# Performance work log

Hardware: AMD Instinct MI355X
Metric: run time of the kernel (lower is better)

Reference implementation:

```python
import jax, jax.numpy as jnp
import numpy as np
from jax import lax

FIELD = 32          # backbone receptive-field stride (field_size of ResNet50)
K = 3               # number of anchor sizes
ANCHOR_PX = (32, 64, 96)
POOL = 2
TILES = 3
NMS_IOU = 0.3
R_POST = 512        # post-NMS proposal cap (static shape for jit)
IMG = 1536
MG = IMG // FIELD   # 48x48 feature map
C = 256
HID = 1024


def setup_inputs() -> dict:
    key = jax.random.key(0)
    ks = jax.random.split(key, 6)
    # create_anchors: per feature cell (grid step FIELD) and per anchor size,
    # row = [x_upper_left, y_upper_left, width, height]
    grid = np.arange(MG, dtype=np.float32) * FIELD + FIELD / 2.0  # cell centers
    cy, cx, aa = np.meshgrid(grid, grid, np.array(ANCHOR_PX, np.float32), indexing='ij')
    anchors = np.stack([cx - aa / 2, cy - aa / 2, aa, aa], axis=-1).reshape(-1, 4).astype(np.float32)
    return {
        'features': jax.random.normal(ks[0], (1, MG, MG, C), jnp.float32),
        'anchors': jnp.asarray(anchors),
        'W_obj': jax.random.normal(ks[1], (C, 2 * K), jnp.float32) * 0.1,
        'b_obj': jnp.zeros((2 * K,), jnp.float32),
        'W_reg': jax.random.normal(ks[2], (C, 4 * K), jnp.float32) * 0.01,
        'b_reg': jnp.zeros((4 * K,), jnp.float32),
        'W_fc1': jax.random.normal(ks[3], (TILES * TILES * C, HID), jnp.float32) * 0.02,
        'b_fc1': jnp.zeros((HID,), jnp.float32),
        'W_fc2': jax.random.normal(ks[4], (HID, 4), jnp.float32) * 0.01,
        'b_fc2': jnp.zeros((4,), jnp.float32),
    }


def _map_outputs(out, anchors):
    # out: [M, N, K*D] RPN output; returns [A, D], one row per anchor
    apx = jnp.asarray(ANCHOR_PX, jnp.int32)
    k = jnp.argmax(anchors[:, 3].astype(jnp.int32)[:, None] == apx[None, :], axis=1)
    px = ((anchors[:, 0] + anchors[:, 2] * 0.5) / FIELD).astype(jnp.int32)
    py = ((anchors[:, 1] + anchors[:, 3] * 0.5) / FIELD).astype(jnp.int32)
    M, N, _ = out.shape
    r = out.reshape(M, N, K, -1)
    return r[py, px, k]


def _unparameterize(reg, anchors):
    cxa = anchors[:, 0] + anchors[:, 2] * 0.5
    cya = anchors[:, 1] + anchors[:, 3] * 0.5
    cx = reg[:, 0] * anchors[:, 2] + cxa
    cy = reg[:, 1] * anchors[:, 3] + cya
    w = anchors[:, 2] * jnp.exp(reg[:, 2])
    h = anchors[:, 3] * jnp.exp(reg[:, 3])
    return jnp.stack([cx - w * 0.5, cy - h * 0.5, w, h], axis=1)


def _clip_boxes(b, W, H):
    x1 = jnp.clip(b[:, 0], 0.0, W)
    y1 = jnp.clip(b[:, 1], 0.0, H)
    x2 = jnp.clip(b[:, 0] + b[:, 2], 0.0, W)
    y2 = jnp.clip(b[:, 1] + b[:, 3], 0.0, H)
    return jnp.stack([x1, y1, x2 - x1, y2 - y1], axis=1)


def _pairwise_iou(b):
    x1, y1 = b[:, 0], b[:, 1]
    x2, y2 = b[:, 0] + b[:, 2], b[:, 1] + b[:, 3]
    iw = jnp.maximum(0.0, jnp.minimum(x2[:, None], x2[None, :]) - jnp.maximum(x1[:, None], x1[None, :]))
    ih = jnp.maximum(0.0, jnp.minimum(y2[:, None], y2[None, :]) - jnp.maximum(y1[:, None], y1[None, :]))
    inter = iw * ih
    area = (x2 - x1) * (y2 - y1)
    return inter / (area[:, None] + area[None, :] - inter + 1e-8)


def _roialign(fmap, boxes):
    # fmap: [M, N, C]; boxes: [R, 4] xywh -> [R, TILES, TILES, C]
    M, N, Cc = fmap.shape
    S = TILES * POOL
    offs = (jnp.arange(S, dtype=boxes.dtype) + 0.5) / S
    fx = jnp.clip((boxes[:, 0:1] + offs[None, :] * boxes[:, 2:3]) / FIELD - 0.5, 0.0, N - 1.0)
    fy = jnp.clip((boxes[:, 1:2] + offs[None, :] * boxes[:, 3:4]) / FIELD - 0.5, 0.0, M - 1.0)
    x0 = jnp.floor(fx).astype(jnp.int32); x1 = jnp.minimum(x0 + 1, N - 1); wx = fx - x0
    y0 = jnp.floor(fy).astype(jnp.int32); y1 = jnp.minimum(y0 + 1, M - 1); wy = fy - y0
    def g(yi, xi):
        return fmap[yi[:, :, None], xi[:, None, :]]  # [R, S, S, C]
    wX = wx[:, None, :, None]; wY = wy[:, :, None, None]
    v = (g(y0, x0) * (1 - wY) * (1 - wX) + g(y0, x1) * (1 - wY) * wX
         + g(y1, x0) * wY * (1 - wX) + g(y1, x1) * wY * wX)
    R = boxes.shape[0]
    return v.reshape(R, TILES, POOL, TILES, POOL, Cc).mean(axis=(2, 4))


def reference(features, anchors, W_obj, b_obj, W_reg, b_reg, W_fc1, b_fc1, W_fc2, b_fc2):
    fmap = features[0]  # [M, N, C]
    out_obj = fmap @ W_obj + b_obj   # [M, N, 2K]
    out_reg = fmap @ W_reg + b_reg   # [M, N, 4K]
    rpn_obj = jax.nn.softmax(_map_outputs(out_obj, anchors), axis=1)  # [A, 2]
    rpn_reg = _map_outputs(out_reg, anchors)                          # [A, 4]
    boxes = _clip_boxes(_unparameterize(rpn_reg, anchors), float(IMG), float(IMG))
    scores = rpn_obj[:, 1]
    A = boxes.shape[0]
    # NMS (sequential greedy suppression on score-sorted boxes)
    order = jnp.argsort(-scores)
    iou_mat = lax.stop_gradient(_pairwise_iou(boxes[order]))  # [A, A], index selection is non-diff
    idx = jnp.arange(A)
    def body(i, keep):
        sup = jnp.any((iou_mat[i] > NMS_IOU) & keep & (idx < i))
        return keep.at[i].set(~sup)
    keep = lax.fori_loop(0, A, body, jnp.zeros((A,), bool))
    masked = jnp.where(keep, scores[order], -1e9)
    _, topi = lax.top_k(masked, R_POST)
    sel = order[topi]
    sel_boxes = boxes[sel]
    sel_obj = rpn_obj[sel]
    pooled = _roialign(fmap, sel_boxes)            # [R, TILES, TILES, C]
    flat = pooled.reshape(R_POST, -1)
    h = jax.nn.relu(flat @ W_fc1 + b_fc1)
    align_reg = h @ W_fc2 + b_fc2                  # [R, 4]
    align_boxes = _unparameterize(align_reg, sel_boxes)
    # concat (rpn_obj, rpn_boxes, align_boxes) -> [R, 10]
    return jnp.concatenate([sel_obj, sel_boxes, align_boxes], axis=1)
```

## Files before the change

kernel.cpp:

```cpp
#include <hip/hip_runtime.h>
#include <hip/hip_bf16.h>

typedef unsigned long long ull;

#define MGRID 48
#define CCH   256
#define NCELL 2304
#define NA    6912
#define NW    108
#define NHID  1024
#define KFC   2304
#define RPOST 512
#define IMGF  1536.0f

typedef __attribute__((ext_vector_type(8))) short short8v;
typedef __attribute__((ext_vector_type(4))) float f32x4;

__global__ __launch_bounds__(256) void rpn_head(const float* __restrict__ feat,
    const float* __restrict__ Wobj, const float* __restrict__ bobj,
    const float* __restrict__ Wreg, const float* __restrict__ breg,
    float* __restrict__ rpn){
  int g = blockIdx.x*256 + threadIdx.x;
  int cell = g / 18, o = g % 18;
  const float* x = feat + cell*CCH;
  const float* W; int stride; float acc;
  if (o < 6){ W = Wobj + o; stride = 6;  acc = bobj[o];   }
  else      { W = Wreg + (o-6); stride = 12; acc = breg[o-6]; }
  #pragma unroll 8
  for (int c=0;c<CCH;++c) acc += x[c]*W[c*stride];
  rpn[cell*18 + o] = acc;
}

__global__ __launch_bounds__(256) void anchor_prep(const float* __restrict__ rpn,
    const float* __restrict__ anchors, float* __restrict__ probs,
    float* __restrict__ boxes, ull* __restrict__ keys){
  int a = blockIdx.x*256 + threadIdx.x;
  int cell = a/3, k = a%3;
  const float* rc = rpn + cell*18;
  float l0 = rc[2*k], l1 = rc[2*k+1];
  float m  = fmaxf(l0,l1);
  float e0 = expf(l0-m), e1 = expf(l1-m);
  float s  = e0 + e1;
  float p0 = e0/s, p1 = e1/s;
  probs[a*2+0] = p0; probs[a*2+1] = p1;
  float4 an = ((const float4*)anchors)[a];
  float r0 = rc[6+4*k+0], r1 = rc[6+4*k+1], r2 = rc[6+4*k+2], r3 = rc[6+4*k+3];
  float cxa = an.x + an.z*0.5f, cya = an.y + an.w*0.5f;
  float cx = r0*an.z + cxa, cy = r1*an.w + cya;
  float w  = an.z*expf(r2),  hh = an.w*expf(r3);
  float bx = cx - w*0.5f, by = cy - hh*0.5f;
  float x1 = fminf(fmaxf(bx,      0.0f), IMGF);
  float y1 = fminf(fmaxf(by,      0.0f), IMGF);
  float x2 = fminf(fmaxf(bx + w,  0.0f), IMGF);
  float y2 = fminf(fmaxf(by + hh, 0.0f), IMGF);
  float4 bo; bo.x = x1; bo.y = y1; bo.z = x2 - x1; bo.w = y2 - y1;
  ((float4*)boxes)[a] = bo;
  keys[a] = ((ull)__float_as_uint(p1) << 32) | (unsigned)(NA-1-a);
}

__global__ __launch_bounds__(256) void rank_part(const ull* __restrict__ keys,
                                                 int* __restrict__ part){
  __shared__ ull lk[256];
  int t = threadIdx.x;
  int ib = blockIdx.x, jb = blockIdx.y;
  lk[t] = keys[jb*256 + t];
  int i = ib*256 + t;
  ull ki = keys[i];
  __syncthreads();
  int cnt = 0;
  #pragma unroll 16
  for (int j=0;j<256;++j) cnt += (lk[j] > ki) ? 1 : 0;
  part[jb*NA + i] = cnt;
}

__global__ __launch_bounds__(256) void rank_scatter(const int* __restrict__ part,
    const float* __restrict__ boxes, int* __restrict__ ord, float* __restrict__ sboxes){
  int i = blockIdx.x*256 + threadIdx.x;
  int r = 0;
  #pragma unroll
  for (int jb=0;jb<27;++jb) r += part[jb*NA + i];
  ord[r] = i;
  ((float4*)sboxes)[r] = ((const float4*)boxes)[i];
}

__global__ __launch_bounds__(256) void iou_mask(const float* __restrict__ sboxes,
                                                ull* __restrict__ maskT){
  int gid = blockIdx.x*256 + threadIdx.x;
  int i = gid % NA;
  int w = gid / NA;
  if ((i >> 6) > w + 1) return;
  float4 bi = ((const float4*)sboxes)[i];
  float x1i = bi.x, y1i = bi.y;
  float x2i = bi.x + bi.z, y2i = bi.y + bi.w;
  float ai  = (x2i - x1i) * (y2i - y1i);
  const float4* bj4 = (const float4*)sboxes + w*64;
  ull bits = 0;
  #pragma unroll 8
  for (int jj=0;jj<64;++jj){
    float4 bj = bj4[jj];
    float x1j = bj.x, y1j = bj.y;
    float x2j = bj.x + bj.z, y2j = bj.y + bj.w;
    float aj  = (x2j - x1j) * (y2j - y1j);
    float iw = fmaxf(fminf(x2i,x2j) - fmaxf(x1i,x1j), 0.0f);
    float ih = fmaxf(fminf(y2i,y2j) - fmaxf(y1i,y1j), 0.0f);
    float inter = iw*ih;
    float den = ai + aj - inter + 1e-8f;
    if (inter > 0.3f*den) bits |= (1ull<<jj);
  }
  maskT[(size_t)w*NA + i] = bits;
}

__global__ __launch_bounds__(256) void nms_wcvt(const ull* __restrict__ maskT,
    const int* __restrict__ ord, const float* __restrict__ sboxes,
    const float* __restrict__ probs, const float* __restrict__ Wfc1,
    ushort* __restrict__ Wt, float* __restrict__ out, float* __restrict__ selb){
  if (blockIdx.x != 0){
    __shared__ float tile[32][33];
    int bid = blockIdx.x - 1;
    int bx = bid & 31;
    int by = bid >> 5;
    int tx = threadIdx.x & 31, ty = threadIdx.x >> 5;
    #pragma unroll
    for (int it=0; it<4; ++it)
      tile[ty + 8*it][tx] = Wfc1[(size_t)(by*32 + ty + 8*it)*NHID + bx*32 + tx];
    __syncthreads();
    #pragma unroll
    for (int it=0; it<4; ++it){
      __hip_bfloat16 b = __float2bfloat16(tile[tx][ty + 8*it]);
      Wt[(size_t)(bx*32 + ty + 8*it)*KFC + by*32 + tx] = *(ushort*)&b;
    }
    return;
  }

  __shared__ ull remv[NW];
  __shared__ ull keepw[NW];
  __shared__ ull kb_sh[2];
  __shared__ int selpos[RPOST];
  __shared__ int base_sh[NW];
  __shared__ int cnt_sh, done_sh;
  int t = threadIdx.x;
  if (t < NW){ remv[t] = 0ull; keepw[t] = 0ull; }
  if (t == 0){ cnt_sh = 0; done_sh = 0; kb_sh[0] = 0ull; kb_sh[1] = 0ull; }
  __syncthreads();

  ull dg_cur = 0, srow_cur = 0, kb_prev = 0;
  if (t < 64) dg_cur = maskT[t];

  for (int c = 0; c < NW; ++c){
    if (t < 64){
      ull dg_nxt = 0, srow_nxt = 0;
      if (c+1 < NW){
        dg_nxt   = maskT[(size_t)(c+1)*NA + (size_t)(c+1)*64 + t];
        srow_nxt = maskT[(size_t)c*NA + (size_t)(c+1)*64 + t];
      }
      ull w0 = remv[c];
      bool dec  = ((w0 >> t) & 1ull) || ((srow_cur & kb_prev) != 0ull);
      bool kept = false;
      ull sup = dg_cur & ((1ull << t) - 1ull);
      for (;;){
        ull K = __ballot(kept);
        ull D = __ballot(dec);
        if (D == ~0ull) break;
        if (!dec){
          if (sup & K)                 { dec = true; }
          else if ((sup & ~D) == 0ull) { dec = true; kept = true; }
        }
      }
      ull kb = __ballot(kept);
      int cnt0 = cnt_sh;
      ull below = kb & ((1ull << t) - 1ull);
      int myrank = cnt0 + __popcll(below);
      if (kept && myrank < RPOST) selpos[myrank] = c*64 + t;
      if (t == 0){
        kb_sh[c & 1] = kb;
        keepw[c] = kb;
        int nc = cnt0 + __popcll(kb);
        if (nc >= RPOST){ nc = RPOST; done_sh = 1; }
        cnt_sh = nc;
      }
      kb_prev = kb; dg_cur = dg_nxt; srow_cur = srow_nxt;
    } else {
      int u = t - 64;
      int wp = c + 1 + u;
      if (c >= 1 && wp < NW){
        ull kbp = kb_sh[(c-1) & 1];
        if (kbp){
          const ull* row = maskT + (size_t)wp*NA + (size_t)(c-1)*64;
          ull acc = remv[wp];
          #pragma unroll
          for (int b=0;b<64;++b)
            acc |= (0ull - ((kbp >> b) & 1ull)) & row[b];
          remv[wp] = acc;
        }
      }
    }
    __syncthreads();
    if (done_sh) break;
  }
  __syncthreads();
  int cnt0 = cnt_sh;
  if (cnt0 < RPOST){
    if (t < NW){
      int s = 0;
      for (int w2=0; w2<t; ++w2) s += __popcll(~keepw[w2]);
      base_sh[t] = s;
    }
    __syncthreads();
    for (int p = t; p < NA; p += 256){
      int w2 = p >> 6, b = p & 63;
      ull kw = keepw[w2];
      if (!((kw >> b) & 1ull)){
        int rank = cnt0 + base_sh[w2] + __popcll(~kw & ((1ull << b) - 1ull));
        if (rank < RPOST) selpos[rank] = p;
      }
    }
  }
  __syncthreads();
  for (int s=t; s<RPOST; s+=256){
    int pos = selpos[s];
    int orig = ord[pos];
    float4 b = ((const float4*)sboxes)[pos];
    out[s*10+0] = probs[orig*2+0];
    out[s*10+1] = probs[orig*2+1];
    out[s*10+2] = b.x; out[s*10+3] = b.y; out[s*10+4] = b.z; out[s*10+5] = b.w;
    ((float4*)selb)[s] = b;
  }
}

__global__ __launch_bounds__(256) void roialign(const float* __restrict__ feat,
    const float* __restrict__ selb, __hip_bfloat16* __restrict__ pooled){
  int r = blockIdx.x, c = threadIdx.x;
  float4 b = ((const float4*)selb)[r];
  int x0[6], x1[6], y0[6], y1[6];
  float wx[6], wy[6];
  #pragma unroll
  for (int s=0;s<6;++s){
    float off = ((float)s + 0.5f) / 6.0f;
    float fx = (b.x + off*b.z) / 32.0f - 0.5f;
    fx = fminf(fmaxf(fx, 0.0f), 47.0f);
    int xx0 = (int)floorf(fx);
    x0[s] = xx0; x1[s] = min(xx0+1, 47); wx[s] = fx - (float)xx0;
    float fy = (b.y + off*b.w) / 32.0f - 0.5f;
    fy = fminf(fmaxf(fy, 0.0f), 47.0f);
    int yy0 = (int)floorf(fy);
    y0[s] = yy0; y1[s] = min(yy0+1, 47); wy[s] = fy - (float)yy0;
  }
  #pragma unroll
  for (int ty=0;ty<3;++ty){
    #pragma unroll
    for (int tx=0;tx<3;++tx){
      float sum = 0.0f;
      #pragma unroll
      for (int py=0;py<2;++py){
        #pragma unroll
        for (int px=0;px<2;++px){
          int sy = ty*2+py, sx = tx*2+px;
          float wxx = wx[sx], wyy = wy[sy];
          float v00 = feat[(y0[sy]*MGRID + x0[sx])*CCH + c];
          float v01 = feat[(y0[sy]*MGRID + x1[sx])*CCH + c];
          float v10 = feat[(y1[sy]*MGRID + x0[sx])*CCH + c];
          float v11 = feat[(y1[sy]*MGRID + x1[sx])*CCH + c];
          sum += v00*(1.0f-wyy)*(1.0f-wxx) + v01*(1.0f-wyy)*wxx
               + v10*wyy*(1.0f-wxx)        + v11*wyy*wxx;
        }
      }
      pooled[((r*9) + ty*3 + tx)*CCH + c] = __float2bfloat16(sum * 0.25f);
    }
  }
}

__global__ __launch_bounds__(256) void fc1_mfma(const ushort* __restrict__ A,
    const ushort* __restrict__ Bt, const float* __restrict__ bias,
    float* __restrict__ Hp){
  __shared__ ushort As[4096];
  __shared__ ushort Bs[4096];
  const int t = threadIdx.x;
  const int bn = blockIdx.x, bm = blockIdx.y, bz = blockIdx.z;
  const int wv = t >> 6, lane = t & 63;
  const int wm = (wv >> 1) * 32, wn = (wv & 1) * 32;

  const int r0 = t >> 3, kc = t & 7;
  const int r1 = r0 + 32;
  const int kbase = bz * 144;
  const float4* gA0 = (const float4*)A  + (size_t)(bm*64 + r0)*288 + kbase + kc;
  const float4* gA1 = (const float4*)A  + (size_t)(bm*64 + r1)*288 + kbase + kc;
  const float4* gB0 = (const float4*)Bt + (size_t)(bn*64 + r0)*288 + kbase + kc;
  const float4* gB1 = (const float4*)Bt + (size_t)(bn*64 + r1)*288 + kbase + kc;
  float4* sA0 = (float4*)As + ((r0<<3) | (kc ^ (r0&7)));
  float4* sA1 = (float4*)As + ((r1<<3) | (kc ^ (r1&7)));
  float4* sB0 = (float4*)Bs + ((r0<<3) | (kc ^ (r0&7)));
  float4* sB1 = (float4*)Bs + ((r1<<3) | (kc ^ (r1&7)));

  const int fr = lane & 15, fkg = lane >> 4;
  const int arow0 = wm + fr,      arow1 = wm + 16 + fr;
  const int brow0 = wn + fr,      brow1 = wn + 16 + fr;

  f32x4 acc00{}, acc01{}, acc10{}, acc11{};

  const int KT = 18;
  float4 pa0 = gA0[0], pa1 = gA1[0], pb0 = gB0[0], pb1 = gB1[0];
  for (int kt = 0; kt < KT; ++kt){
    __syncthreads();
    *sA0 = pa0; *sA1 = pa1; *sB0 = pb0; *sB1 = pb1;
    if (kt + 1 < KT){
      pa0 = gA0[(kt+1)*8]; pa1 = gA1[(kt+1)*8];
      pb0 = gB0[(kt+1)*8]; pb1 = gB1[(kt+1)*8];
    }
    __syncthreads();
    #pragma unroll
    for (int kk2 = 0; kk2 < 2; ++kk2){
      int kidx = fkg + kk2*4;
      short8v a0 = *(const short8v*)(As + ((((arow0<<3) | (kidx ^ (arow0&7)))) << 3));
      short8v a1 = *(const short8v*)(As + ((((arow1<<3) | (kidx ^ (arow1&7)))) << 3));
      short8v b0 = *(const short8v*)(Bs + ((((brow0<<3) | (kidx ^ (brow0&7)))) << 3));
      short8v b1 = *(const short8v*)(Bs + ((((brow1<<3) | (kidx ^ (brow1&7)))) << 3));
      acc00 = __builtin_amdgcn_mfma_f32_16x16x32_bf16(a0, b0, acc00, 0, 0, 0);
      acc01 = __builtin_amdgcn_mfma_f32_16x16x32_bf16(a0, b1, acc01, 0, 0, 0);
      acc10 = __builtin_amdgcn_mfma_f32_16x16x32_bf16(a1, b0, acc10, 0, 0, 0);
      acc11 = __builtin_amdgcn_mfma_f32_16x16x32_bf16(a1, b1, acc11, 0, 0, 0);
    }
  }
  float* H = Hp + (size_t)bz * 512 * NHID;
  const int orow = bm*64 + wm + (lane>>4)*4;
  const int ocol = bn*64 + wn + (lane&15);
  #pragma unroll
  for (int i=0;i<2;++i){
    #pragma unroll
    for (int j=0;j<2;++j){
      f32x4 a = (i==0) ? ((j==0)?acc00:acc01) : ((j==0)?acc10:acc11);
      #pragma unroll
      for (int reg=0;reg<4;++reg){
        int row = orow + i*16 + reg;
        int col = ocol + j*16;
        float v = a[reg] + (bz == 0 ? bias[col] : 0.0f);
        H[(size_t)row*NHID + col] = v;
      }
    }
  }
}

__global__ __launch_bounds__(64) void fc2(const float* __restrict__ h0,
    const float* __restrict__ h1, const float* __restrict__ W2,
    const float* __restrict__ b2, const float* __restrict__ selb,
    float* __restrict__ out){
  int r = blockIdx.x, lane = threadIdx.x;
  float a0=0,a1=0,a2=0,a3=0;
  #pragma unroll 4
  for (int it=0; it<16; ++it){
    int k = it*64 + lane;
    float hv = fmaxf(h0[(size_t)r*NHID + k] + h1[(size_t)r*NHID + k], 0.0f);
    float4 w = ((const float4*)W2)[k];
    a0 += hv*w.x; a1 += hv*w.y; a2 += hv*w.z; a3 += hv*w.w;
  }
  #pragma unroll
  for (int off=32; off>0; off>>=1){
    a0 += __shfl_down(a0, off);
    a1 += __shfl_down(a1, off);
    a2 += __shfl_down(a2, off);
    a3 += __shfl_down(a3, off);
  }
  if (lane == 0){
    float4 b = ((const float4*)selb)[r];
    float r0 = a0 + b2[0], r1 = a1 + b2[1], r2 = a2 + b2[2], r3 = a3 + b2[3];
    float cxa = b.x + b.z*0.5f, cya = b.y + b.w*0.5f;
    float cx = r0*b.z + cxa, cy = r1*b.w + cya;
    float w  = b.z*expf(r2),  hh = b.w*expf(r3);
    out[r*10+6] = cx - w*0.5f;
    out[r*10+7] = cy - hh*0.5f;
    out[r*10+8] = w;
    out[r*10+9] = hh;
  }
}

extern "C" void kernel_launch(void* const* d_in, const int* in_sizes, int n_in,
                              void* d_out, int out_size, void* d_ws, size_t ws_size,
                              hipStream_t stream) {
  const float* feat    = (const float*)d_in[0];
  const float* anchors = (const float*)d_in[1];
  const float* Wobj    = (const float*)d_in[2];
  const float* bobj    = (const float*)d_in[3];
  const float* Wreg    = (const float*)d_in[4];
  const float* breg    = (const float*)d_in[5];
  const float* Wfc1    = (const float*)d_in[6];
  const float* bfc1    = (const float*)d_in[7];
  const float* Wfc2    = (const float*)d_in[8];
  const float* bfc2    = (const float*)d_in[9];
  float* out = (float*)d_out;
  char* ws = (char*)d_ws;

  float* rpn    = (float*)(ws + 0);
  float* probs  = (float*)(ws + 165888);
  float* boxes  = (float*)(ws + 221184);
  ull*   keys   = (ull*)  (ws + 331776);
  int*   ord    = (int*)  (ws + 387072);
  float* sboxes = (float*)(ws + 414720);
  int*   part   = (int*)  (ws + 525312);
  ull*   maskT  = (ull*)  (ws + 1271808);
  float* selb   = (float*)(ws + 7243776);
  __hip_bfloat16* pooled = (__hip_bfloat16*)(ws + 7251968);
  float* h      = (float*)(ws + 9611264);
  ushort* Wt    = (ushort*)(ws + 13805568);

  float* h0 = h;
  float* h1 = h + 512*NHID;

  hipLaunchKernelGGL(rpn_head,     dim3(162),     dim3(256), 0, stream, feat, Wobj, bobj, Wreg, breg, rpn);
  hipLaunchKernelGGL(anchor_prep,  dim3(27),      dim3(256), 0, stream, rpn, anchors, probs, boxes, keys);
  hipLaunchKernelGGL(rank_part,    dim3(27,27),   dim3(256), 0, stream, keys, part);
  hipLaunchKernelGGL(rank_scatter, dim3(27),      dim3(256), 0, stream, part, boxes, ord, sboxes);
  hipLaunchKernelGGL(iou_mask,     dim3(2916),    dim3(256), 0, stream, sboxes, maskT);
  hipLaunchKernelGGL(nms_wcvt,     dim3(2305),    dim3(256), 0, stream, maskT, ord, sboxes, probs, Wfc1, Wt, out, selb);
  hipLaunchKernelGGL(roialign,     dim3(512),     dim3(256), 0, stream, feat, selb, pooled);
  hipLaunchKernelGGL(fc1_mfma,     dim3(16,8,2),  dim3(256), 0, stream, (const ushort*)pooled, Wt, bfc1, h);
  hipLaunchKernelGGL(fc2,          dim3(512),     dim3(64),  0, stream, h0, h1, Wfc2, bfc2, selb, out);
}
```

Baseline: 92.25 us.

## Move W_fc1 conversion into RPN head, compact IoU grid, vectorize RPN loads

The fp32-to-bf16 transpose of W_fc1 moves out of the NMS kernel and into extra blocks of the first RPN-head kernel, so the single-block NMS runs alone instead of competing with 2304 conversion blocks. The IoU mask kernel now launches only the triangular band of (word, row-block) pairs it needs. It recovers the indices through a sqrt-based inverse with correction loops, which removes the blocks that used to launch and exit early. The RPN head reads features as float4. The conversion now sits on the path before anchor prep, adding work to the early stages.

```diff
diff --git a/kernel.cpp b/kernel.cpp
--- a/kernel.cpp
+++ b/kernel.cpp
@@ -16,18 +16,42 @@
 typedef __attribute__((ext_vector_type(8))) short short8v;
 typedef __attribute__((ext_vector_type(4))) float f32x4;
 
-__global__ __launch_bounds__(256) void rpn_head(const float* __restrict__ feat,
+__global__ __launch_bounds__(256) void rpn_wcvt(const float* __restrict__ feat,
     const float* __restrict__ Wobj, const float* __restrict__ bobj,
     const float* __restrict__ Wreg, const float* __restrict__ breg,
-    float* __restrict__ rpn){
+    float* __restrict__ rpn, const float* __restrict__ Wfc1,
+    ushort* __restrict__ Wt){
+  if (blockIdx.x >= 162){
+    __shared__ float tile[32][33];
+    int bid = blockIdx.x - 162;
+    int bx = bid & 31;
+    int by = bid >> 5;
+    int tx = threadIdx.x & 31, ty = threadIdx.x >> 5;
+    #pragma unroll
+    for (int it=0; it<4; ++it)
+      tile[ty + 8*it][tx] = Wfc1[(size_t)(by*32 + ty + 8*it)*NHID + bx*32 + tx];
+    __syncthreads();
+    #pragma unroll
+    for (int it=0; it<4; ++it){
+      __hip_bfloat16 b = __float2bfloat16(tile[tx][ty + 8*it]);
+      Wt[(size_t)(bx*32 + ty + 8*it)*KFC + by*32 + tx] = *(ushort*)&b;
+    }
+    return;
+  }
   int g = blockIdx.x*256 + threadIdx.x;
   int cell = g / 18, o = g % 18;
-  const float* x = feat + cell*CCH;
   const float* W; int stride; float acc;
   if (o < 6){ W = Wobj + o; stride = 6;  acc = bobj[o];   }
   else      { W = Wreg + (o-6); stride = 12; acc = breg[o-6]; }
-  #pragma unroll 8
-  for (int c=0;c<CCH;++c) acc += x[c]*W[c*stride];
+  const float4* x4 = (const float4*)(feat + cell*CCH);
+  #pragma unroll 4
+  for (int c4=0;c4<CCH/4;++c4){
+    float4 xv = x4[c4];
+    acc += xv.x*W[(4*c4+0)*stride];
+    acc += xv.y*W[(4*c4+1)*stride];
+    acc += xv.z*W[(4*c4+2)*stride];
+    acc += xv.w*W[(4*c4+3)*stride];
+  }
   rpn[cell*18 + o] = acc;
 }
 
@@ -83,12 +107,18 @@
   ((float4*)sboxes)[r] = ((const float4*)boxes)[i];
 }
 
+#define NQ 5993
 __global__ __launch_bounds__(256) void iou_mask(const float* __restrict__ sboxes,
                                                 ull* __restrict__ maskT){
-  int gid = blockIdx.x*256 + threadIdx.x;
-  int i = gid % NA;
-  int w = gid / NA;
-  if ((i >> 6) > w + 1) return;
+  int g = blockIdx.x*256 + threadIdx.x;
+  int q = g >> 6;
+  if (q >= NQ) return;
+  int w = (int)((sqrtf(8.0f*(float)q + 9.0f) - 3.0f) * 0.5f);
+  if (w > 107) w = 107;
+  while (w < 107 && (w+1)*(w+4)/2 <= q) ++w;
+  while (w > 0 && w*(w+3)/2 > q) --w;
+  int ib = q - w*(w+3)/2;
+  int i = ib*64 + (g & 63);
   float4 bi = ((const float4*)sboxes)[i];
   float x1i = bi.x, y1i = bi.y;
   float x2i = bi.x + bi.z, y2i = bi.y + bi.w;
@@ -110,28 +140,10 @@
   maskT[(size_t)w*NA + i] = bits;
 }
 
-__global__ __launch_bounds__(256) void nms_wcvt(const ull* __restrict__ maskT,
+__global__ __launch_bounds__(256) void nms(const ull* __restrict__ maskT,
     const int* __restrict__ ord, const float* __restrict__ sboxes,
-    const float* __restrict__ probs, const float* __restrict__ Wfc1,
-    ushort* __restrict__ Wt, float* __restrict__ out, float* __restrict__ selb){
-  if (blockIdx.x != 0){
-    __shared__ float tile[32][33];
-    int bid = blockIdx.x - 1;
-    int bx = bid & 31;
-    int by = bid >> 5;
-    int tx = threadIdx.x & 31, ty = threadIdx.x >> 5;
-    #pragma unroll
-    for (int it=0; it<4; ++it)
-      tile[ty + 8*it][tx] = Wfc1[(size_t)(by*32 + ty + 8*it)*NHID + bx*32 + tx];
-    __syncthreads();
-    #pragma unroll
-    for (int it=0; it<4; ++it){
-      __hip_bfloat16 b = __float2bfloat16(tile[tx][ty + 8*it]);
-      Wt[(size_t)(bx*32 + ty + 8*it)*KFC + by*32 + tx] = *(ushort*)&b;
-    }
-    return;
-  }
-
+    const float* __restrict__ probs, float* __restrict__ out,
+    float* __restrict__ selb){
   __shared__ ull remv[NW];
   __shared__ ull keepw[NW];
   __shared__ ull kb_sh[2];
@@ -404,12 +416,12 @@
   float* h0 = h;
   float* h1 = h + 512*NHID;
 
-  hipLaunchKernelGGL(rpn_head,     dim3(162),     dim3(256), 0, stream, feat, Wobj, bobj, Wreg, breg, rpn);
+  hipLaunchKernelGGL(rpn_wcvt,     dim3(2466),    dim3(256), 0, stream, feat, Wobj, bobj, Wreg, breg, rpn, Wfc1, Wt);
   hipLaunchKernelGGL(anchor_prep,  dim3(27),      dim3(256), 0, stream, rpn, anchors, probs, boxes, keys);
   hipLaunchKernelGGL(rank_part,    dim3(27,27),   dim3(256), 0, stream, keys, part);
   hipLaunchKernelGGL(rank_scatter, dim3(27),      dim3(256), 0, stream, part, boxes, ord, sboxes);
-  hipLaunchKernelGGL(iou_mask,     dim3(2916),    dim3(256), 0, stream, sboxes, maskT);
-  hipLaunchKernelGGL(nms_wcvt,     dim3(2305),    dim3(256), 0, stream, maskT, ord, sboxes, probs, Wfc1, Wt, out, selb);
+  hipLaunchKernelGGL(iou_mask,     dim3(1499),    dim3(256), 0, stream, sboxes, maskT);
+  hipLaunchKernelGGL(nms,          dim3(1),       dim3(256), 0, stream, maskT, ord, sboxes, probs, out, selb);
   hipLaunchKernelGGL(roialign,     dim3(512),     dim3(256), 0, stream, feat, selb, pooled);
   hipLaunchKernelGGL(fc1_mfma,     dim3(16,8,2),  dim3(256), 0, stream, (const ushort*)pooled, Wt, bfc1, h);
   hipLaunchKernelGGL(fc2,          dim3(512),     dim3(64),  0, stream, h0, h1, Wfc2, bfc2, selb, out);
```

After: 91.21 us. No clear change (-1.1%).
